# Optimization experiments

Measured on AMD Instinct MI355X. Metric: run time of the kernel, lower is better.

## Reference

```python
import jax, jax.numpy as jnp
import numpy as np

N_HEAD = 8

def setup_inputs() -> dict:
    key = jax.random.key(0)
    ks = jax.random.split(key, 5)
    B, T, C = 2, 4096, 512
    x = jax.random.normal(ks[0], (B, T, C), dtype=jnp.float32)
    w_attn = jax.random.normal(ks[1], (3 * C, C), dtype=jnp.float32) * (1.0 / np.sqrt(C))
    b_attn = jax.random.normal(ks[2], (3 * C,), dtype=jnp.float32) * 0.02
    w_proj = jax.random.normal(ks[3], (C, C), dtype=jnp.float32) * (1.0 / np.sqrt(C))
    b_proj = jax.random.normal(ks[4], (C,), dtype=jnp.float32) * 0.02
    return {"x": x, "w_attn": w_attn, "b_attn": b_attn, "w_proj": w_proj, "b_proj": b_proj}

def reference(x, w_attn, b_attn, w_proj, b_proj):
    B, T, C = x.shape
    H = N_HEAD
    D = C // H  # head dim
    qkv = x @ w_attn.T + b_attn  # [B,T,3C]
    q, k, v = jnp.split(qkv, 3, axis=-1)
    # b t (h d) -> b h t d
    def to_heads(t):
        return t.reshape(B, T, H, D).transpose(0, 2, 1, 3)
    q, k, v = to_heads(q), to_heads(k), to_heads(v)
    scale = 1.0 / np.sqrt(D).astype(np.float32)
    att = jnp.einsum('bhqd,bhkd->bhqk', q, k) * scale  # [B,H,T,T]
    causal = jnp.tril(jnp.ones((T, T), dtype=bool))
    att = jnp.where(causal[None, None], att, jnp.float32(-jnp.inf))
    att = jax.nn.softmax(att, axis=-1)
    y = jnp.einsum('bhqk,bhkd->bhqd', att, v)  # [B,H,T,D]
    y = y.transpose(0, 2, 1, 3).reshape(B, T, C)
    return y @ w_proj.T + b_proj
```

## Files before the change

kernel.cpp:

```cpp
#include <hip/hip_runtime.h>

typedef __attribute__((ext_vector_type(8))) __bf16 bf16x8;
typedef __attribute__((ext_vector_type(4))) __bf16 bf16x4;
typedef __attribute__((ext_vector_type(4))) float f32x4;
typedef __attribute__((ext_vector_type(16))) float f32x16;
typedef __attribute__((ext_vector_type(4))) unsigned uint32x4;

#define AS1 __attribute__((address_space(1)))
#define AS3 __attribute__((address_space(3)))

#if __has_builtin(__builtin_amdgcn_exp2f)
#define EXP2(x) __builtin_amdgcn_exp2f(x)
#else
#define EXP2(x) exp2f(x)
#endif

#define QSCALE 0.18033688011112042f

#define N_X 4194304
#define N_WA 786432
#define N_WP 262144
__global__ __launch_bounds__(256) void convert_all_k(const float* __restrict__ x,
                                                     const float* __restrict__ wa,
                                                     const float* __restrict__ wp,
                                                     __bf16* __restrict__ xb,
                                                     __bf16* __restrict__ wab,
                                                     __bf16* __restrict__ wpb) {
  int i = (blockIdx.x * 256 + threadIdx.x) * 4;
  const float* src;
  __bf16* dst;
  int off;
  if (i < N_X)              { src = x;  dst = xb;  off = i; }
  else if (i < N_X + N_WA)  { src = wa; dst = wab; off = i - N_X; }
  else if (i < N_X + N_WA + N_WP) { src = wp; dst = wpb; off = i - N_X - N_WA; }
  else return;
  float4 v = *reinterpret_cast<const float4*>(src + off);
  bf16x4 o;
  o[0] = (__bf16)v.x; o[1] = (__bf16)v.y; o[2] = (__bf16)v.z; o[3] = (__bf16)v.w;
  *reinterpret_cast<bf16x4*>(dst + off) = o;
}

template <int EPI>
__global__ __launch_bounds__(256) void gemm_bt(const __bf16* __restrict__ A,
                                               const __bf16* __restrict__ Bm,
                                               const float* __restrict__ bias,
                                               void* __restrict__ outp,
                                               __bf16* __restrict__ vtout,
                                               int M, int N, int K) {
  __shared__ __bf16 a_lds[128 * 64];
  __shared__ __bf16 b_lds[128 * 64];
  const int tid = threadIdx.x;
  const int lane = tid & 63;
  const int w = tid >> 6;
  const int wm = w >> 1, wn = w & 1;
  const int ll = lane & 15, lh = lane >> 4;
  const int bid = (int)blockIdx.x;
  const int NT = N >> 7;
  const int xcd = bid & 7, lidx = bid >> 3;
  const int m0 = (xcd * 8 + lidx / NT) * 128;
  const int n0 = (lidx % NT) * 128;
  f32x4 acc[4][4] = {};

  for (int k0 = 0; k0 < K; k0 += 64) {
    __syncthreads();
#pragma unroll
    for (int i = 0; i < 4; ++i) {
      int ch = i * 256 + w * 64 + lane;
      int r = ch >> 3, c8 = ch & 7;
      const __bf16* ga = A + (size_t)(m0 + r) * K + k0 + c8 * 8;
      __builtin_amdgcn_global_load_lds((const AS1 void*)ga,
                                       (AS3 void*)(a_lds + (i * 256 + w * 64) * 8), 16, 0, 0);
      const __bf16* gb = Bm + (size_t)(n0 + r) * K + k0 + c8 * 8;
      __builtin_amdgcn_global_load_lds((const AS1 void*)gb,
                                       (AS3 void*)(b_lds + (i * 256 + w * 64) * 8), 16, 0, 0);
    }
    __syncthreads();
#pragma unroll
    for (int kc = 0; kc < 2; ++kc) {
      bf16x8 af[4], bfr[4];
#pragma unroll
      for (int m = 0; m < 4; ++m)
        af[m] = *reinterpret_cast<const bf16x8*>(a_lds + (wm * 64 + m * 16 + ll) * 64 + kc * 32 + lh * 8);
#pragma unroll
      for (int n = 0; n < 4; ++n)
        bfr[n] = *reinterpret_cast<const bf16x8*>(b_lds + (wn * 64 + n * 16 + ll) * 64 + kc * 32 + lh * 8);
#pragma unroll
      for (int m = 0; m < 4; ++m)
#pragma unroll
        for (int n = 0; n < 4; ++n)
          acc[m][n] = __builtin_amdgcn_mfma_f32_16x16x32_bf16(af[m], bfr[n], acc[m][n], 0, 0, 0);
    }
  }
  if (EPI == 1) {
#pragma unroll
    for (int m = 0; m < 4; ++m) {
      int gm = m0 + wm * 64 + m * 16 + lh * 4;
#pragma unroll
      for (int n = 0; n < 4; ++n) {
        int gn = n0 + wn * 64 + n * 16 + ll;
        float bs = bias[gn];
#pragma unroll
        for (int r = 0; r < 4; ++r)
          ((float*)outp)[(size_t)(gm + r) * N + gn] = acc[m][n][r] + bs;
      }
    }
  } else if (n0 < 1024) {
    __syncthreads();
    __bf16* tb = (w < 2 ? a_lds : b_lds) + (w & 1) * 4096;
    const float sc = (n0 < 512) ? (float)QSCALE : 1.0f;
#pragma unroll
    for (int m = 0; m < 4; ++m)
#pragma unroll
      for (int n = 0; n < 4; ++n) {
        float bs = bias[n0 + wn * 64 + n * 16 + ll];
#pragma unroll
        for (int r = 0; r < 4; ++r)
          tb[(m * 16 + lh * 4 + r) * 64 + n * 16 + ll] = (__bf16)((acc[m][n][r] + bs) * sc);
      }
    const int rsub = lane >> 3, csub = (lane & 7) * 8;
#pragma unroll
    for (int i = 0; i < 8; ++i) {
      bf16x8 vv = *reinterpret_cast<const bf16x8*>(tb + (i * 8 + rsub) * 64 + csub);
      *reinterpret_cast<bf16x8*>((__bf16*)outp +
          (size_t)(m0 + wm * 64 + i * 8 + rsub) * N + n0 + wn * 64 + csub) = vv;
    }
  } else {
#pragma unroll
    for (int m = 0; m < 4; ++m) {
      int gm = m0 + wm * 64 + m * 16 + lh * 4;
#pragma unroll
      for (int n = 0; n < 4; ++n) {
        int gn = n0 + wn * 64 + n * 16 + ll;
        float bs = bias[gn];
        bf16x4 pk;
#pragma unroll
        for (int r = 0; r < 4; ++r) pk[r] = (__bf16)(acc[m][n][r] + bs);
        *reinterpret_cast<bf16x4*>(vtout + ((size_t)((gm >> 12) * 512 + (gn - 1024))) * 4096 + (gm & 4095)) = pk;
      }
    }
  }
}

struct Tbl { unsigned short t[204]; };
constexpr Tbl build_tbl() {
  Tbl T{};
  int sizes[204] = {};
  int n = 0;
  for (int p = 0; p < 2; ++p)
    for (int qx = 0; qx < 32; ++qx) {
      int total = 2 * qx + 2;
      int nch = (total + 11) / 12;
      int cum = 0;
      for (int q = 0; q < qx; ++q) cum += (2 * q + 13) / 12;
      for (int c = 0; c < nch; ++c) {
        int sz = total - 12 * c; if (sz > 12) sz = 12;
        T.t[n] = (unsigned short)(qx | (c << 5) | (p << 8) | ((cum + c) << 9));
        sizes[n] = sz;
        ++n;
      }
    }
  for (int i = 1; i < n; ++i) {
    unsigned short tv = T.t[i]; int sv = sizes[i];
    int j = i - 1;
    while (j >= 0 && sizes[j] < sv) { T.t[j + 1] = T.t[j]; sizes[j + 1] = sizes[j]; --j; }
    T.t[j + 1] = tv; sizes[j + 1] = sv;
  }
  return T;
}
__device__ __constant__ Tbl g_tbl = build_tbl();

__device__ inline unsigned cvtpk(float lo, float hi_) {
  unsigned r;
  asm("v_cvt_pk_bf16_f32 %0, %1, %2" : "=v"(r) : "v"(lo), "v"(hi_));
  return r;
}

__global__ __launch_bounds__(256, 4) void attn_k(const __bf16* __restrict__ qkv,
                                                 const __bf16* __restrict__ vt,
                                                 __bf16* __restrict__ opart,
                                                 float* __restrict__ lpart,
                                                 __bf16* __restrict__ y) {
  __shared__ __bf16 k_lds[2][64 * 64];
  __shared__ __bf16 v_lds[2][64 * 64];
  const int tid = threadIdx.x, lane = tid & 63, w = tid >> 6;
  const int hi = lane >> 5, q31 = lane & 31;
  const int swz = q31 & 7;

  const int bid = (int)blockIdx.x;
  const int e = g_tbl.t[bid >> 3];
  const int qx = e & 31, c = (e >> 5) & 7, p = (e >> 8) & 1, j = e >> 9;
  const int bh = (bid & 7) * 2 + p;
  const int pslot = bh * 102 + j;
  const int b = bh >> 3, h = bh & 7;
  const int q0 = qx * 128;
  const int qw0 = q0 + w * 32;
  const int t0 = 12 * c;
  const int t1 = min(12 * c + 12, 2 * qx + 2);

  const __bf16* qp = qkv + (size_t)b * 4096 * 1536 + h * 64;
  const __bf16* kp = qp + 512;
  const __bf16* vtp = vt + (size_t)(b * 512 + h * 64) * 4096;

  bf16x8 qf[4];
  {
    const __bf16* qr = qp + (size_t)(qw0 + q31) * 1536 + hi * 8;
#pragma unroll
    for (int d = 0; d < 4; ++d) qf[d] = *reinterpret_cast<const bf16x8*>(qr + d * 16);
  }

  f32x16 o0 = {}, o1 = {};
  float l_run = 0.f;

  auto stage = [&](int tt, int ss) {
    const int kv0s = tt * 64;
#pragma unroll
    for (int i = 0; i < 2; ++i) {
      int ch = i * 256 + tid;
      int r = ch >> 3, cc = ch & 7;
      int cs = cc ^ (r & 7);
      __builtin_amdgcn_global_load_lds(
          (const AS1 void*)(kp + (size_t)(kv0s + r) * 1536 + cs * 8),
          (AS3 void*)(&k_lds[ss][(i * 256 + w * 64) * 8]), 16, 0, 0);
      __builtin_amdgcn_global_load_lds(
          (const AS1 void*)(vtp + (size_t)r * 4096 + kv0s + cs * 8),
          (AS3 void*)(&v_lds[ss][(i * 256 + w * 64) * 8]), 16, 0, 0);
    }
  };

  stage(t0, 0);
  __builtin_amdgcn_sched_barrier(0);

  int slot = 0;
  for (int t = t0; t < t1; ++t) {
    asm volatile("s_waitcnt vmcnt(0)" ::: "memory");
    __builtin_amdgcn_sched_barrier(0);
    __builtin_amdgcn_s_barrier();
    __builtin_amdgcn_sched_barrier(0);
    if (t + 1 < t1) {
      stage(t + 1, slot ^ 1);
      __builtin_amdgcn_sched_barrier(0);
    }
    const int kv0 = t * 64;
    if (kv0 <= qw0 + 31) {
      f32x16 s0 = {}, s1 = {};
      __builtin_amdgcn_s_setprio(1);
#pragma unroll
      for (int d = 0; d < 4; ++d) {
        int c0 = ((d * 2 + hi) ^ swz) * 8;
        s0 = __builtin_amdgcn_mfma_f32_32x32x16_bf16(
            *reinterpret_cast<const bf16x8*>(&k_lds[slot][q31 * 64 + c0]), qf[d], s0, 0, 0, 0);
        s1 = __builtin_amdgcn_mfma_f32_32x32x16_bf16(
            *reinterpret_cast<const bf16x8*>(&k_lds[slot][(32 + q31) * 64 + c0]), qf[d], s1, 0, 0, 0);
      }
      __builtin_amdgcn_s_setprio(0);
      if (kv0 + 63 > qw0) {
        const int q = qw0 + q31;
#pragma unroll
        for (int r = 0; r < 16; ++r) {
          int crow = (r & 3) + 8 * (r >> 2) + 4 * hi;
          if (kv0 + crow > q) s0[r] = -1e30f;
          if (kv0 + 32 + crow > q) s1[r] = -1e30f;
        }
      }
#pragma unroll
      for (int r = 0; r < 16; ++r) s0[r] = EXP2(s0[r]);
#pragma unroll
      for (int r = 0; r < 16; ++r) s1[r] = EXP2(s1[r]);
      {
        float a8[8];
#pragma unroll
        for (int r = 0; r < 8; ++r)
          a8[r] = (s0[r] + s0[r + 8]) + (s1[r] + s1[r + 8]);
        l_run += (((a8[0] + a8[1]) + (a8[2] + a8[3])) + ((a8[4] + a8[5]) + (a8[6] + a8[7])));
      }
      uint32x4 pa[4];
#pragma unroll
      for (int half = 0; half < 2; ++half) {
        const int bse = half * 8;
        {
          unsigned x1 = cvtpk(s0[bse + 0], s0[bse + 1]);
          unsigned y1 = cvtpk(s0[bse + 4], s0[bse + 5]);
          asm("v_permlane32_swap_b32 %0, %1" : "+v"(x1), "+v"(y1));
          pa[half][0] = x1; pa[half][2] = y1;
          unsigned x2 = cvtpk(s0[bse + 2], s0[bse + 3]);
          unsigned y2 = cvtpk(s0[bse + 6], s0[bse + 7]);
          asm("v_permlane32_swap_b32 %0, %1" : "+v"(x2), "+v"(y2));
          pa[half][1] = x2; pa[half][3] = y2;
        }
        {
          unsigned x1 = cvtpk(s1[bse + 0], s1[bse + 1]);
          unsigned y1 = cvtpk(s1[bse + 4], s1[bse + 5]);
          asm("v_permlane32_swap_b32 %0, %1" : "+v"(x1), "+v"(y1));
          pa[2 + half][0] = x1; pa[2 + half][2] = y1;
          unsigned x2 = cvtpk(s1[bse + 2], s1[bse + 3]);
          unsigned y2 = cvtpk(s1[bse + 6], s1[bse + 7]);
          asm("v_permlane32_swap_b32 %0, %1" : "+v"(x2), "+v"(y2));
          pa[2 + half][1] = x2; pa[2 + half][3] = y2;
        }
      }
      __builtin_amdgcn_s_setprio(1);
#pragma unroll
      for (int ks = 0; ks < 4; ++ks) {
        int c0 = ((ks * 2 + hi) ^ swz) * 8;
        bf16x8 pfrag = __builtin_bit_cast(bf16x8, pa[ks]);
        o0 = __builtin_amdgcn_mfma_f32_32x32x16_bf16(
            *reinterpret_cast<const bf16x8*>(&v_lds[slot][q31 * 64 + c0]), pfrag, o0, 0, 0, 0);
        o1 = __builtin_amdgcn_mfma_f32_32x32x16_bf16(
            *reinterpret_cast<const bf16x8*>(&v_lds[slot][(32 + q31) * 64 + c0]), pfrag, o1, 0, 0, 0);
      }
      __builtin_amdgcn_s_setprio(0);
    }
    __builtin_amdgcn_sched_barrier(0);
    slot ^= 1;
  }

  l_run += __shfl_xor(l_run, 32);

  const int rloc = w * 32 + q31;
  if (t0 == 0 && t1 == 2 * qx + 2) {
    const float inv = 1.f / l_run;
    __bf16* yr = y + ((size_t)b * 4096 + qw0 + q31) * 512 + h * 64;
#pragma unroll
    for (int g = 0; g < 4; ++g) {
      bf16x4 v0, v1;
#pragma unroll
      for (int jj = 0; jj < 4; ++jj) {
        v0[jj] = (__bf16)(o0[g * 4 + jj] * inv);
        v1[jj] = (__bf16)(o1[g * 4 + jj] * inv);
      }
      *reinterpret_cast<bf16x4*>(yr + 8 * g + 4 * hi) = v0;
      *reinterpret_cast<bf16x4*>(yr + 32 + 8 * g + 4 * hi) = v1;
    }
  } else {
    __bf16* ob = opart + ((size_t)pslot * 128 + rloc) * 64;
#pragma unroll
    for (int g = 0; g < 4; ++g) {
      bf16x4 v0, v1;
#pragma unroll
      for (int jj = 0; jj < 4; ++jj) {
        v0[jj] = (__bf16)(o0[g * 4 + jj]);
        v1[jj] = (__bf16)(o1[g * 4 + jj]);
      }
      *reinterpret_cast<bf16x4*>(ob + 8 * g + 4 * hi) = v0;
      *reinterpret_cast<bf16x4*>(ob + 32 + 8 * g + 4 * hi) = v1;
    }
    if (hi == 0) lpart[pslot * 128 + rloc] = l_run;
  }
}

__global__ __launch_bounds__(256) void combine_k(const __bf16* __restrict__ opart,
                                                 const float* __restrict__ lpart,
                                                 __bf16* __restrict__ y) {
  const int bid = (int)blockIdx.x;
  const int bh = bid >> 5, qx = bid & 31;
  if (qx < 6) return;
  const int b = bh >> 3, h = bh & 7;
  const int n = (2 * qx + 13) / 12;
  int cum = 0;
  for (int q = 0; q < qx; ++q) cum += (2 * q + 13) / 12;
  const int g0 = bh * 102 + cum;
  const int tid = threadIdx.x;
  const int r = tid >> 1, dh = (tid & 1) * 32;

  float W = 0.f;
  float acc[32] = {};
  for (int i = 0; i < n; ++i) {
    W += lpart[(g0 + i) * 128 + r];
    const __bf16* op = opart + ((size_t)(g0 + i) * 128 + r) * 64 + dh;
#pragma unroll
    for (int jj = 0; jj < 4; ++jj) {
      bf16x8 v = *reinterpret_cast<const bf16x8*>(op + jj * 8);
#pragma unroll
      for (int e = 0; e < 8; ++e) acc[jj * 8 + e] += (float)v[e];
    }
  }
  const float inv = 1.f / W;
  __bf16* yr = y + ((size_t)b * 4096 + qx * 128 + r) * 512 + h * 64 + dh;
#pragma unroll
  for (int jj = 0; jj < 4; ++jj) {
    bf16x8 ov;
#pragma unroll
    for (int e = 0; e < 8; ++e) ov[e] = (__bf16)(acc[jj * 8 + e] * inv);
    *reinterpret_cast<bf16x8*>(yr + jj * 8) = ov;
  }
}

extern "C" void kernel_launch(void* const* d_in, const int* in_sizes, int n_in,
                              void* d_out, int out_size, void* d_ws, size_t ws_size,
                              hipStream_t stream) {
  const float* x      = (const float*)d_in[0];
  const float* w_attn = (const float*)d_in[1];
  const float* b_attn = (const float*)d_in[2];
  const float* w_proj = (const float*)d_in[3];
  const float* b_proj = (const float*)d_in[4];
  float* out = (float*)d_out;

  const int Bv = 2, T = 4096, C = 512;
  const int M = Bv * T;

  const size_t NPART = (size_t)1632 * 128 * 64;
  __bf16* opart  = (__bf16*)d_ws;
  __bf16* x_bf   = opart;
  __bf16* wa_bf  = opart + NPART;
  __bf16* wp_bf  = wa_bf + (size_t)786432;
  __bf16* qkv_bf = wp_bf + (size_t)262144;
  __bf16* y_bf   = qkv_bf + (size_t)12582912;
  __bf16* vt_bf  = y_bf + (size_t)4194304;
  float*  lpart  = (float*)(vt_bf + (size_t)4194304);

  const int ntot = N_X + N_WA + N_WP;
  convert_all_k<<<(ntot / 4 + 255) / 256, 256, 0, stream>>>(x, w_attn, w_proj, x_bf, wa_bf, wp_bf);

  gemm_bt<0><<<dim3((3 * C / 128) * (M / 128)), 256, 0, stream>>>(x_bf, wa_bf, b_attn, qkv_bf, vt_bf, M, 3 * C, C);
  attn_k<<<dim3(1632), 256, 0, stream>>>(qkv_bf, vt_bf, opart, lpart, y_bf);
  combine_k<<<dim3(512), 256, 0, stream>>>(opart, lpart, y_bf);
  gemm_bt<1><<<dim3((C / 128) * (M / 128)), 256, 0, stream>>>(y_bf, wp_bf, b_proj, out, nullptr, M, C, C);
}
```

Before: 113.0 us.

## Triple-buffer K tiles and prefetch K two iterations ahead of V

Splits the combined K/V staging into separate K and V loaders. K now uses three LDS buffers and is prefetched two tiles ahead, while V stays double-buffered. The per-iteration wait becomes vmcnt(2), so the next K tile can still be in flight while the current tile is computed. Global addresses are precomputed once and advanced by pointer increments instead of recomputed each stage. The extra 8 KB of LDS per block may limit occupancy, and short ranges issue one unused K prefetch.

Result: no change. 113.0 us (+0.0%).

```diff
diff --git a/kernel.cpp b/kernel.cpp
--- a/kernel.cpp
+++ b/kernel.cpp
@@ -180,7 +180,7 @@
                                                  __bf16* __restrict__ opart,
                                                  float* __restrict__ lpart,
                                                  __bf16* __restrict__ y) {
-  __shared__ __bf16 k_lds[2][64 * 64];
+  __shared__ __bf16 k_lds[3][64 * 64];
   __shared__ __bf16 v_lds[2][64 * 64];
   const int tid = threadIdx.x, lane = tid & 63, w = tid >> 6;
   const int hi = lane >> 5, q31 = lane & 31;
@@ -198,8 +198,12 @@
   const int t1 = min(12 * c + 12, 2 * qx + 2);
 
   const __bf16* qp = qkv + (size_t)b * 4096 * 1536 + h * 64;
-  const __bf16* kp = qp + 512;
   const __bf16* vtp = vt + (size_t)(b * 512 + h * 64) * 4096;
+
+  const int rr = tid >> 3;
+  const int cs = (tid & 7) ^ (rr & 7);
+  const __bf16* kg = qp + 512 + (size_t)(t0 * 64 + rr) * 1536 + cs * 8;
+  const __bf16* vg = vtp + (size_t)rr * 4096 + t0 * 64 + cs * 8;
 
   bf16x8 qf[4];
   {
@@ -211,34 +215,43 @@
   f32x16 o0 = {}, o1 = {};
   float l_run = 0.f;
 
-  auto stage = [&](int tt, int ss) {
-    const int kv0s = tt * 64;
-#pragma unroll
-    for (int i = 0; i < 2; ++i) {
-      int ch = i * 256 + tid;
-      int r = ch >> 3, cc = ch & 7;
-      int cs = cc ^ (r & 7);
-      __builtin_amdgcn_global_load_lds(
-          (const AS1 void*)(kp + (size_t)(kv0s + r) * 1536 + cs * 8),
-          (AS3 void*)(&k_lds[ss][(i * 256 + w * 64) * 8]), 16, 0, 0);
-      __builtin_amdgcn_global_load_lds(
-          (const AS1 void*)(vtp + (size_t)r * 4096 + kv0s + cs * 8),
-          (AS3 void*)(&v_lds[ss][(i * 256 + w * 64) * 8]), 16, 0, 0);
-    }
+  auto stageK = [&](int ks) {
+    __builtin_amdgcn_global_load_lds((const AS1 void*)kg,
+        (AS3 void*)(&k_lds[ks][w * 512]), 16, 0, 0);
+    __builtin_amdgcn_global_load_lds((const AS1 void*)(kg + 32 * 1536),
+        (AS3 void*)(&k_lds[ks][2048 + w * 512]), 16, 0, 0);
+    kg += 64 * 1536;
   };
-
-  stage(t0, 0);
+  auto stageV = [&](int vs) {
+    __builtin_amdgcn_global_load_lds((const AS1 void*)vg,
+        (AS3 void*)(&v_lds[vs][w * 512]), 16, 0, 0);
+    __builtin_amdgcn_global_load_lds((const AS1 void*)(vg + 32 * 4096),
+        (AS3 void*)(&v_lds[vs][2048 + w * 512]), 16, 0, 0);
+    vg += 64;
+  };
+
+  stageV(0);
   __builtin_amdgcn_sched_barrier(0);
-
-  int slot = 0;
+  stageK(0);
+  __builtin_amdgcn_sched_barrier(0);
+  stageK(1);
+  __builtin_amdgcn_sched_barrier(0);
+
+  int kslot = 0, vslot = 0;
   for (int t = t0; t < t1; ++t) {
-    asm volatile("s_waitcnt vmcnt(0)" ::: "memory");
+    if (t + 1 < t1) asm volatile("s_waitcnt vmcnt(2)" ::: "memory");
+    else            asm volatile("s_waitcnt vmcnt(0)" ::: "memory");
     __builtin_amdgcn_sched_barrier(0);
     __builtin_amdgcn_s_barrier();
     __builtin_amdgcn_sched_barrier(0);
     if (t + 1 < t1) {
-      stage(t + 1, slot ^ 1);
+      stageV(vslot ^ 1);
       __builtin_amdgcn_sched_barrier(0);
+      if (t + 2 < t1) {
+        int k2 = kslot + 2; if (k2 >= 3) k2 -= 3;
+        stageK(k2);
+        __builtin_amdgcn_sched_barrier(0);
+      }
     }
     const int kv0 = t * 64;
     if (kv0 <= qw0 + 31) {
@@ -248,9 +261,9 @@
       for (int d = 0; d < 4; ++d) {
         int c0 = ((d * 2 + hi) ^ swz) * 8;
         s0 = __builtin_amdgcn_mfma_f32_32x32x16_bf16(
-            *reinterpret_cast<const bf16x8*>(&k_lds[slot][q31 * 64 + c0]), qf[d], s0, 0, 0, 0);
+            *reinterpret_cast<const bf16x8*>(&k_lds[kslot][q31 * 64 + c0]), qf[d], s0, 0, 0, 0);
         s1 = __builtin_amdgcn_mfma_f32_32x32x16_bf16(
-            *reinterpret_cast<const bf16x8*>(&k_lds[slot][(32 + q31) * 64 + c0]), qf[d], s1, 0, 0, 0);
+            *reinterpret_cast<const bf16x8*>(&k_lds[kslot][(32 + q31) * 64 + c0]), qf[d], s1, 0, 0, 0);
       }
       __builtin_amdgcn_s_setprio(0);
       if (kv0 + 63 > qw0) {
@@ -304,14 +317,15 @@
         int c0 = ((ks * 2 + hi) ^ swz) * 8;
         bf16x8 pfrag = __builtin_bit_cast(bf16x8, pa[ks]);
         o0 = __builtin_amdgcn_mfma_f32_32x32x16_bf16(
-            *reinterpret_cast<const bf16x8*>(&v_lds[slot][q31 * 64 + c0]), pfrag, o0, 0, 0, 0);
+            *reinterpret_cast<const bf16x8*>(&v_lds[vslot][q31 * 64 + c0]), pfrag, o0, 0, 0, 0);
         o1 = __builtin_amdgcn_mfma_f32_32x32x16_bf16(
-            *reinterpret_cast<const bf16x8*>(&v_lds[slot][(32 + q31) * 64 + c0]), pfrag, o1, 0, 0, 0);
+            *reinterpret_cast<const bf16x8*>(&v_lds[vslot][(32 + q31) * 64 + c0]), pfrag, o1, 0, 0, 0);
       }
       __builtin_amdgcn_s_setprio(0);
     }
     __builtin_amdgcn_sched_barrier(0);
-    slot ^= 1;
+    kslot = (kslot == 2) ? 0 : kslot + 1;
+    vslot ^= 1;
   }
 
   l_run += __shfl_xor(l_run, 32);
```
